# Kernel tuning notes

Measured on AMD Instinct MI355X. Metric: run time of the kernel, lower is better.

The kernel has to match this reference:

```python
import jax, jax.numpy as jnp
import numpy as np

EMBED_DIM = 1024
NUM_HEADS = 16
HEAD_DIM = EMBED_DIM // NUM_HEADS
GLOBAL_HEADS = 1
LOCAL_K = 128
SCALE = HEAD_DIM ** -0.5


def setup_inputs() -> dict:
    key = jax.random.key(0)
    ks = jax.random.split(key, 9)
    B, n = 4, 2048
    s = 1.0 / np.sqrt(EMBED_DIM)  # torch Linear default uniform(-1/sqrt(in), 1/sqrt(in))
    def lin(k):
        kw, kb = jax.random.split(k)
        W = jax.random.uniform(kw, (EMBED_DIM, EMBED_DIM), jnp.float32, -s, s)
        b = jax.random.uniform(kb, (EMBED_DIM,), jnp.float32, -s, s)
        return W, b
    wq, bq = lin(ks[0])
    wk, bk = lin(ks[1])
    wv, bv = lin(ks[2])
    wo, bo = lin(ks[3])
    x = jax.random.normal(ks[4], (B, n, EMBED_DIM), jnp.float32)
    return {"x": x, "wq": wq, "bq": bq, "wk": wk, "bk": bk,
            "wv": wv, "bv": bv, "wo": wo, "bo": bo}


def _attend(x, wq, bq, wk, bk, wv, bv, wo, bo):
    B, n, E = x.shape
    H, D = NUM_HEADS, HEAD_DIM
    def proj(W, b):
        t = x @ W.T + b                       # [B, n, E]
        return t.reshape(B, n, H, D).transpose(0, 2, 1, 3)  # [B, H, n, D]
    q, k, v = proj(wq, bq), proj(wk, bk), proj(wv, bv)
    scores = jnp.einsum('bhqd,bhkd->bhqk', q, k) * SCALE  # [B, H, n, n]
    idx = jnp.arange(n)
    band = jnp.abs(idx[:, None] - idx[None, :]) <= LOCAL_K  # [n, n] True = allowed
    is_global = jnp.arange(H) < GLOBAL_HEADS
    mask = band[None, :, :] | is_global[:, None, None]      # [H, n, n]
    scores = jnp.where(mask[None], scores, -jnp.inf)
    attn = jax.nn.softmax(scores, axis=-1)   # dropout is identity (p=0 / eval)
    out = jnp.einsum('bhqk,bhkd->bhqd', attn, v)
    out = out.transpose(0, 2, 1, 3).reshape(B, n, E)
    return out @ wo.T + bo


def reference(x, wq, bq, wk, bk, wv, bv, wo, bo):
    return _attend(x, wq, bq, wk, bk, wv, bv, wo, bo)
```

## Files before the change

### kernel.cpp

```cpp
#include <hip/hip_runtime.h>

typedef __attribute__((ext_vector_type(4))) float f32x4;
typedef __attribute__((ext_vector_type(16))) float f32x16;
typedef __attribute__((ext_vector_type(8))) short s16x8;

#define GLDS(gsrc, ldst) \
  __builtin_amdgcn_global_load_lds((const __attribute__((address_space(1))) void*)(gsrc), \
                                   (__attribute__((address_space(3))) void*)(ldst), 16, 0, 0)

__device__ __forceinline__ ushort f2bf(float f) {
  union { float f; unsigned u; } x; x.f = f;
  unsigned r = (x.u + 0x7FFFu + ((x.u >> 16) & 1u)) >> 16;
  return (ushort)r;
}

__device__ __forceinline__ float fexp2(float x) {
  float r;
  asm("v_exp_f32 %0, %1" : "=v"(r) : "v"(x));
  return r;
}

__device__ __forceinline__ uint cvtpk(float a, float b) {
  uint r;
  asm("v_cvt_pk_bf16_f32 %0, %1, %2" : "=v"(r) : "v"(a), "v"(b));
  return r;
}

__device__ __forceinline__ s16x8 mk_frag(uint x0, uint x1, uint x2, uint x3) {
  union { uint u[4]; s16x8 v; } t;
  t.u[0] = x0; t.u[1] = x1; t.u[2] = x2; t.u[3] = x3;
  return t.v;
}

__global__ __launch_bounds__(256) void castall(
    const float* __restrict__ x, const float* __restrict__ wq, const float* __restrict__ wk,
    const float* __restrict__ wv, const float* __restrict__ wo,
    ushort* __restrict__ xb, ushort* __restrict__ wqkvb, ushort* __restrict__ wob) {
  int bid = blockIdx.x;
  const float* in; ushort* op;
  if (bid < 8192)       { in = x;  op = xb; }
  else if (bid < 9216)  { in = wq; op = wqkvb;           bid -= 8192; }
  else if (bid < 10240) { in = wk; op = wqkvb + 1048576; bid -= 9216; }
  else if (bid < 11264) { in = wv; op = wqkvb + 2097152; bid -= 10240; }
  else                  { in = wo; op = wob;             bid -= 11264; }
  int i = (bid * 256 + threadIdx.x) * 4;
  float4 v = *(const float4*)(in + i);
  ushort4 r;
  r.x = f2bf(v.x); r.y = f2bf(v.y); r.z = f2bf(v.z); r.w = f2bf(v.w);
  *(ushort4*)(op + i) = r;
}

template<int OUTBF16>
__global__ __launch_bounds__(512, 2) void gemm256(
    const ushort* __restrict__ A, const ushort* __restrict__ Bt,
    const float* __restrict__ bias0, const float* __restrict__ bias1,
    const float* __restrict__ bias2,
    void* __restrict__ Cout, int M, int N, int K, int nxn)
{
  __shared__ __align__(16) ushort lds[73728];
  const int tid = threadIdx.x;
  const int w = tid >> 6, lane = tid & 63;
  const int lrow = lane & 15, lg = lane >> 4;
  const int wm = w >> 2, wn = w & 3;
  const int cpx = gridDim.x >> 3;
  const int wgid = ((int)blockIdx.x & 7) * cpx + ((int)blockIdx.x >> 3);
  const int mblk = (wgid / nxn) * 128;
  const int nblk = (wgid % nxn) * 256;
  const int NT = K >> 6;

  const int srow = tid >> 3;
  const int scol = 8 * ((tid & 7) ^ (srow & 7));
  const ushort* Abase = A + (size_t)(mblk + srow) * K + scol;
  const ushort* Bbase = Bt + (size_t)(nblk + srow) * K + scol;
  const size_t rstep = (size_t)64 * K;
  const int dA = w * 512;
  const int dB = 8192 + w * 512;

#define STAGE_A(p, bf) { \
    GLDS((p),         &lds[(bf) + dA]); \
    GLDS((p) + rstep, &lds[(bf) + dA + 4096]); }
#define STAGE_B(p, bf) { \
    GLDS((p),             &lds[(bf) + dB]); \
    GLDS((p) + rstep,     &lds[(bf) + dB + 4096]); \
    GLDS((p) + 2 * rstep, &lds[(bf) + dB + 8192]); \
    GLDS((p) + 3 * rstep, &lds[(bf) + dB + 12288]); }

  const int laneA0 = (wm * 64 + lrow) * 64 + ((lg ^ (lrow & 7)) << 3);
  const int laneA1 = (wm * 64 + lrow) * 64 + (((4 + lg) ^ (lrow & 7)) << 3);
  const int laneB0 = 8192 + (wn * 64 + lrow) * 64 + ((lg ^ (lrow & 7)) << 3);
  const int laneB1 = 8192 + (wn * 64 + lrow) * 64 + (((4 + lg) ^ (lrow & 7)) << 3);

  const f32x4 zero = {0.f, 0.f, 0.f, 0.f};
  f32x4 acc[4][4];
#pragma unroll
  for (int m = 0; m < 4; m++)
#pragma unroll
    for (int n = 0; n < 4; n++) acc[m][n] = zero;

  STAGE_A(Abase, 0); STAGE_B(Bbase, 0);
  if (NT > 1) { STAGE_A(Abase + 64, 24576); STAGE_B(Bbase + 64, 24576); }

  const ushort* aP = Abase + 128;
  const ushort* bP = Bbase + 128;
  int bb = 0, bbS = 49152;

  for (int t = 0; t < NT; ++t) {
    if (t < NT - 1) { asm volatile("s_waitcnt vmcnt(6)" ::: "memory"); }
    else            { asm volatile("s_waitcnt vmcnt(0)" ::: "memory"); }
    __builtin_amdgcn_s_barrier();
    const int pA0 = bb + laneA0, pA1 = bb + laneA1;
    const int pB0 = bb + laneB0, pB1 = bb + laneB1;
    const bool pf = (t + 2 < NT);

    if (pf) STAGE_A(aP, bbS);
    {
      s16x8 af[4], bf_[4];
#pragma unroll
      for (int m = 0; m < 4; m++) af[m] = *(const s16x8*)&lds[pA0 + m * 1024];
#pragma unroll
      for (int n = 0; n < 4; n++) bf_[n] = *(const s16x8*)&lds[pB0 + n * 1024];
      __builtin_amdgcn_s_setprio(1);
#pragma unroll
      for (int m = 0; m < 4; m++)
#pragma unroll
        for (int n = 0; n < 4; n++)
          acc[m][n] = __builtin_amdgcn_mfma_f32_16x16x32_bf16(af[m], bf_[n], acc[m][n], 0, 0, 0);
      __builtin_amdgcn_s_setprio(0);
    }
    if (pf) STAGE_B(bP, bbS);
    {
      s16x8 af[4], bf_[4];
#pragma unroll
      for (int m = 0; m < 4; m++) af[m] = *(const s16x8*)&lds[pA1 + m * 1024];
#pragma unroll
      for (int n = 0; n < 4; n++) bf_[n] = *(const s16x8*)&lds[pB1 + n * 1024];
      __builtin_amdgcn_s_setprio(1);
#pragma unroll
      for (int m = 0; m < 4; m++)
#pragma unroll
        for (int n = 0; n < 4; n++)
          acc[m][n] = __builtin_amdgcn_mfma_f32_16x16x32_bf16(af[m], bf_[n], acc[m][n], 0, 0, 0);
      __builtin_amdgcn_s_setprio(0);
    }
    if (pf) { aP += 64; bP += 64; }
    bb  = (bb  == 49152) ? 0 : bb + 24576;
    bbS = (bbS == 49152) ? 0 : bbS + 24576;
  }
#undef STAGE_A
#undef STAGE_B

  float bias_n[4];
#pragma unroll
  for (int n = 0; n < 4; n++) {
    const int col = nblk + wn * 64 + n * 16 + lrow;
    if (bias1) bias_n[n] = (col < 1024) ? bias0[col]
                          : (col < 2048 ? bias1[col - 1024] : bias2[col - 2048]);
    else bias_n[n] = bias0[col];
  }

  __syncthreads();

  if (OUTBF16) {
    ushort* Ct = lds;
#pragma unroll
    for (int m = 0; m < 4; m++)
#pragma unroll
      for (int n = 0; n < 4; n++)
#pragma unroll
        for (int i = 0; i < 4; i++)
          Ct[(wm * 64 + m * 16 + 4 * lg + i) * 256 + wn * 64 + n * 16 + lrow] =
              f2bf(acc[m][n][i] + bias_n[n]);
    __syncthreads();
    ushort* Cg = (ushort*)Cout;
#pragma unroll
    for (int r = 0; r < 8; r++) {
      const int row = r * 16 + (tid >> 5);
      const int col = (tid & 31) * 8;
      *(s16x8*)&Cg[(size_t)(mblk + row) * N + nblk + col] = *(const s16x8*)&lds[r * 4096 + tid * 8];
    }
  } else {
    float* Cf = (float*)lds;
#pragma unroll
    for (int m = 0; m < 4; m++)
#pragma unroll
      for (int n = 0; n < 4; n++)
#pragma unroll
        for (int i = 0; i < 4; i++)
          Cf[(wm * 64 + m * 16 + 4 * lg + i) * 256 + wn * 64 + n * 16 + lrow] =
              acc[m][n][i] + bias_n[n];
    __syncthreads();
    float* Cg = (float*)Cout;
#pragma unroll
    for (int r = 0; r < 16; r++) {
      const int row = r * 8 + (tid >> 6);
      const int col = (tid & 63) * 4;
      *(float4*)&Cg[(size_t)(mblk + row) * N + nblk + col] = *(const float4*)&Cf[r * 2048 + tid * 4];
    }
  }
}

__global__ __launch_bounds__(128, 2) void attn_kernel(const ushort* __restrict__ qkv,
                                                      ushort* __restrict__ outp,
                                                      float* __restrict__ oPart,
                                                      float* __restrict__ mPart,
                                                      float* __restrict__ lPart)
{
  __shared__ __align__(16) ushort Ks[2][4096];
  __shared__ __align__(16) ushort Vt[2][4096];

  const int tid = threadIdx.x;
  const int w = tid >> 6, lane = tid & 63;
  const int lq = lane & 31, hi = lane >> 5;

  const int bid = (blockIdx.x & 7) * 368 + (blockIdx.x >> 3);
  int h, b, bx, kv_lo, kv_hi, chunk = 0;
  bool isGlobal;
  if (bid < 1024) {
    isGlobal = true; h = 0;
    chunk = bid >> 7;
    int qb = bid & 127;
    b = qb >> 5; bx = qb & 31;
    kv_lo = chunk * 256; kv_hi = kv_lo + 256;
  } else {
    isGlobal = false;
    int t = bid - 1024;
    h = 1 + (t >> 7);
    int qb = t & 127;
    b = qb >> 5; bx = qb & 31;
    kv_lo = bx * 64 - 128; if (kv_lo < 0) kv_lo = 0;
    kv_hi = bx * 64 + 192; if (kv_hi > 2048) kv_hi = 2048;
  }
  const int q0b = bx * 64;
  const int q0w = q0b + w * 32;
  const int q_abs = q0w + lq;
  const ushort* Qp = qkv + (size_t)b * 2048 * 3072 + h * 64;
  const ushort* Kp = Qp + 1024;
  const ushort* Vp = Qp + 2048;

  s16x8 qf[4];
#pragma unroll
  for (int c = 0; c < 4; c++)
    qf[c] = *(const s16x8*)(Qp + (size_t)q_abs * 3072 + 16 * c + 8 * hi);

  f32x16 o0, o1;
#pragma unroll
  for (int r = 0; r < 16; r++) { o0[r] = 0.f; o1[r] = 0.f; }
  float mrun = -3e38f, lsum = 0.f;
  const float SCL = 0.18033688011112042f;

  const int kr = tid >> 3, kc = tid & 7;
  const int vsp = tid >> 3, vsg = tid & 7;
  const int kswz = 8 * (kc ^ (kr & 7));

  const ushort* vr0 = Vp + (size_t)(kv_lo + 4 * vsp) * 3072 + 8 * vsg;
  s16x8 v0 = *(const s16x8*)vr0;
  s16x8 v1 = *(const s16x8*)(vr0 + 3072);
  s16x8 v2 = *(const s16x8*)(vr0 + 6144);
  s16x8 v3 = *(const s16x8*)(vr0 + 9216);
#pragma unroll
  for (int i = 0; i < 4; i++)
    GLDS(Kp + (size_t)(kv_lo + 16 * i + kr) * 3072 + kswz, &Ks[0][i * 1024 + w * 512]);

  int buf = 0;
  for (int kv = kv_lo; kv < kv_hi; kv += 64) {
    const bool needMask = !isGlobal && (kv < q0b - 64 || kv + 64 > q0b + 128);
    const bool hasNext = (kv + 64 < kv_hi);

    s16x8 vn0, vn1, vn2, vn3;
    if (hasNext) {
      const ushort* vr = Vp + (size_t)(kv + 64 + 4 * vsp) * 3072 + 8 * vsg;
      vn0 = *(const s16x8*)vr;
      vn1 = *(const s16x8*)(vr + 3072);
      vn2 = *(const s16x8*)(vr + 6144);
      vn3 = *(const s16x8*)(vr + 9216);
    }

#pragma unroll
    for (int j = 0; j < 8; j++) {
      const int d = 8 * vsg + j;
      const int sl = ((vsp >> 1) ^ j ^ vsg) & 7;
      const int a0 = d * 64 + sl * 8 + ((4 * vsp) & 7);
      *(uint*)&Vt[buf][a0]     = (uint)(ushort)v0[j] | ((uint)(ushort)v1[j] << 16);
      *(uint*)&Vt[buf][a0 + 2] = (uint)(ushort)v2[j] | ((uint)(ushort)v3[j] << 16);
    }
    if (hasNext) asm volatile("s_waitcnt vmcnt(4)" ::: "memory");
    else         asm volatile("s_waitcnt vmcnt(0)" ::: "memory");
    asm volatile("s_waitcnt lgkmcnt(0)" ::: "memory");
    __builtin_amdgcn_s_barrier();
    if (hasNext) {
#pragma unroll
      for (int i = 0; i < 4; i++)
        GLDS(Kp + (size_t)(kv + 64 + 16 * i + kr) * 3072 + kswz, &Ks[buf ^ 1][i * 1024 + w * 512]);
    }

    f32x16 s0, s1;
#pragma unroll
    for (int r = 0; r < 16; r++) { s0[r] = 0.f; s1[r] = 0.f; }
#pragma unroll
    for (int c = 0; c < 4; c++) {
      const int gx = ((2 * c + hi) ^ (lq & 7)) << 3;
      s16x8 kf0 = *(const s16x8*)&Ks[buf][lq * 64 + gx];
      s16x8 kf1 = *(const s16x8*)&Ks[buf][(32 + lq) * 64 + gx];
      s0 = __builtin_amdgcn_mfma_f32_32x32x16_bf16(kf0, qf[c], s0, 0, 0, 0);
      s1 = __builtin_amdgcn_mfma_f32_32x32x16_bf16(kf1, qf[c], s1, 0, 0, 0);
    }

    float rm = -3e38f;
    if (needMask) {
#pragma unroll
      for (int r = 0; r < 16; r++) {
        const int kvr = kv + (r & 3) + 8 * (r >> 2) + 4 * hi;
        const int dq0 = q_abs - kvr;
        s0[r] = (dq0 <= 128 && dq0 >= -128) ? s0[r] : -3e38f;
        const int dq1 = dq0 - 32;
        s1[r] = (dq1 <= 128 && dq1 >= -128) ? s1[r] : -3e38f;
        rm = fmaxf(rm, fmaxf(s0[r], s1[r]));
      }
    } else {
#pragma unroll
      for (int r = 0; r < 16; r++) rm = fmaxf(rm, fmaxf(s0[r], s1[r]));
    }
    rm = fmaxf(rm, __shfl_xor(rm, 32)) * SCL;

    if (!__all(rm <= mrun + 8.f)) {
      float mnew = fmaxf(mrun, rm);
      float alpha = fexp2(mrun - mnew);
      mrun = mnew;
      lsum *= alpha;
#pragma unroll
      for (int r = 0; r < 16; r++) {
        float av = __shfl(alpha, (r & 3) + 8 * (r >> 2) + 4 * hi);
        o0[r] *= av; o1[r] *= av;
      }
    }

    float rs = 0.f;
#pragma unroll
    for (int r = 0; r < 16; r++) {
      s0[r] = fexp2(__builtin_fmaf(s0[r], SCL, -mrun)); rs += s0[r];
      s1[r] = fexp2(__builtin_fmaf(s1[r], SCL, -mrun)); rs += s1[r];
    }
    rs += __shfl_xor(rs, 32);
    lsum += rs;

#pragma unroll
    for (int cc = 0; cc < 4; cc++) {
      uint x0, x1, x2, x3;
      if (cc == 0) { x0 = cvtpk(s0[0], s0[1]);  x1 = cvtpk(s0[2], s0[3]);
                     x2 = cvtpk(s0[4], s0[5]);  x3 = cvtpk(s0[6], s0[7]); }
      else if (cc == 1) { x0 = cvtpk(s0[8], s0[9]);   x1 = cvtpk(s0[10], s0[11]);
                          x2 = cvtpk(s0[12], s0[13]); x3 = cvtpk(s0[14], s0[15]); }
      else if (cc == 2) { x0 = cvtpk(s1[0], s1[1]);  x1 = cvtpk(s1[2], s1[3]);
                          x2 = cvtpk(s1[4], s1[5]);  x3 = cvtpk(s1[6], s1[7]); }
      else { x0 = cvtpk(s1[8], s1[9]);   x1 = cvtpk(s1[10], s1[11]);
             x2 = cvtpk(s1[12], s1[13]); x3 = cvtpk(s1[14], s1[15]); }
      uint t0 = hi ? x0 : x2;
      uint t1 = hi ? x1 : x3;
      uint r0 = __shfl_xor(t0, 32);
      uint r1 = __shfl_xor(t1, 32);
      uint w0 = hi ? r0 : x0;
      uint w1 = hi ? r1 : x1;
      uint w2 = hi ? x2 : r0;
      uint w3 = hi ? x3 : r1;
      s16x8 pa = mk_frag(w0, w1, w2, w3);
#pragma unroll
      for (int db = 0; db < 2; db++) {
        const int d = 32 * db + lq;
        s16x8 vf = *(const s16x8*)&Vt[buf][d * 64 +
            ((((2 * cc + hi) ^ (d & 7) ^ (d >> 3)) & 7) << 3)];
        if (db == 0) o0 = __builtin_amdgcn_mfma_f32_32x32x16_bf16(pa, vf, o0, 0, 0, 0);
        else         o1 = __builtin_amdgcn_mfma_f32_32x32x16_bf16(pa, vf, o1, 0, 0, 0);
      }
    }

    v0 = vn0; v1 = vn1; v2 = vn2; v3 = vn3;
    buf ^= 1;
  }

  if (isGlobal) {
    const size_t rq = (size_t)(chunk * 4 + b) * 2048 + q0w;
    if (hi == 0) {
      mPart[rq + lq] = mrun;
      lPart[rq + lq] = lsum;
    }
#pragma unroll
    for (int r = 0; r < 16; r++) {
      const int qr = (r & 3) + 8 * (r >> 2) + 4 * hi;
      oPart[(rq + qr) * 64 + lq]      = o0[r];
      oPart[(rq + qr) * 64 + 32 + lq] = o1[r];
    }
  } else {
    float linv = 1.f / lsum;
#pragma unroll
    for (int r = 0; r < 16; r++) {
      const int qr = (r & 3) + 8 * (r >> 2) + 4 * hi;
      float iv = __shfl(linv, qr);
      size_t orow = (size_t)(b * 2048 + q0w + qr) * 1024 + h * 64;
      outp[orow + lq]      = f2bf(o0[r] * iv);
      outp[orow + 32 + lq] = f2bf(o1[r] * iv);
    }
  }
}

__global__ __launch_bounds__(256) void combine_kernel(const float* __restrict__ oPart,
                                                      const float* __restrict__ mPart,
                                                      const float* __restrict__ lPart,
                                                      ushort* __restrict__ attno) {
  const int tid = threadIdx.x;
  const int row = blockIdx.x * 64 + (tid >> 2);
  const int d0 = (tid & 3) * 16;
  float m[8], l[8], M = -3e38f;
#pragma unroll
  for (int p = 0; p < 8; p++) {
    m[p] = mPart[p * 8192 + row];
    l[p] = lPart[p * 8192 + row];
    M = fmaxf(M, m[p]);
  }
  float L = 0.f, wgt[8];
#pragma unroll
  for (int p = 0; p < 8; p++) { wgt[p] = fexp2(m[p] - M); L += wgt[p] * l[p]; }
  float inv = 1.f / L;
  float acc[16];
#pragma unroll
  for (int j = 0; j < 16; j++) acc[j] = 0.f;
#pragma unroll
  for (int p = 0; p < 8; p++) {
    const float* op = oPart + ((size_t)p * 8192 + row) * 64 + d0;
    float wv = wgt[p];
#pragma unroll
    for (int j = 0; j < 16; j += 4) {
      float4 v = *(const float4*)(op + j);
      acc[j]     += wv * v.x; acc[j + 1] += wv * v.y;
      acc[j + 2] += wv * v.z; acc[j + 3] += wv * v.w;
    }
  }
  ushort* dst = attno + (size_t)row * 1024 + d0;
#pragma unroll
  for (int j = 0; j < 16; j++) dst[j] = f2bf(acc[j] * inv);
}

extern "C" void kernel_launch(void* const* d_in, const int* in_sizes, int n_in,
                              void* d_out, int out_size, void* d_ws, size_t ws_size,
                              hipStream_t stream) {
  const float* x  = (const float*)d_in[0];
  const float* wq = (const float*)d_in[1];
  const float* bq = (const float*)d_in[2];
  const float* wk = (const float*)d_in[3];
  const float* bk = (const float*)d_in[4];
  const float* wv = (const float*)d_in[5];
  const float* bv = (const float*)d_in[6];
  const float* wo = (const float*)d_in[7];
  const float* bo = (const float*)d_in[8];

  char* ws = (char*)d_ws;
  ushort* xb    = (ushort*)(ws);
  ushort* wqkvb = (ushort*)(ws + 16777216);
  ushort* wob   = (ushort*)(ws + 23068672);
  ushort* qkvb  = (ushort*)(ws + 25165824);
  ushort* attno = (ushort*)(ws + 75497472);
  float* oPart = (float*)(ws);
  float* mPart = (float*)(ws + 16777216);
  float* lPart = (float*)(ws + 16777216 + 262144);

  castall<<<12288, 256, 0, stream>>>(x, wq, wk, wv, wo, xb, wqkvb, wob);

  gemm256<1><<<768, 512, 0, stream>>>(xb, wqkvb, bq, bk, bv,
                                      (void*)qkvb, 8192, 3072, 1024, 12);

  attn_kernel<<<2944, 128, 0, stream>>>(qkvb, attno, oPart, mPart, lPart);
  combine_kernel<<<128, 256, 0, stream>>>(oPart, mPart, lPart, attno);

  gemm256<0><<<256, 512, 0, stream>>>(attno, wob, bo, nullptr, nullptr,
                                      (void*)d_out, 8192, 1024, 1024, 4);
}
```

Baseline: 159.0 us.

## Grow attention block to 128 queries with 4 waves sharing K/V tiles

The attention kernel now uses 256-thread blocks covering 128 query rows (four waves of 32) instead of 64, halving the grid. Each K/V tile staged in LDS is shared by twice as many queries, which cuts redundant global loads and LDS staging per query. Waves skip the compute for KV tiles outside their own band window via a per-wave active flag. The trade-off is that the union band per block is wider (384 keys), so some waves idle at barriers while others compute, and occupancy per CU changes with the larger blocks.

```diff
diff --git a/kernel.cpp b/kernel.cpp
--- a/kernel.cpp
+++ b/kernel.cpp
@@ -199,7 +199,7 @@
   }
 }
 
-__global__ __launch_bounds__(128, 2) void attn_kernel(const ushort* __restrict__ qkv,
+__global__ __launch_bounds__(256, 2) void attn_kernel(const ushort* __restrict__ qkv,
                                                       ushort* __restrict__ outp,
                                                       float* __restrict__ oPart,
                                                       float* __restrict__ mPart,
@@ -211,28 +211,29 @@
   const int tid = threadIdx.x;
   const int w = tid >> 6, lane = tid & 63;
   const int lq = lane & 31, hi = lane >> 5;
-
-  const int bid = (blockIdx.x & 7) * 368 + (blockIdx.x >> 3);
+  const float NINF = -__builtin_inff();
+
+  const int bid = (blockIdx.x & 7) * 184 + (blockIdx.x >> 3);
   int h, b, bx, kv_lo, kv_hi, chunk = 0;
   bool isGlobal;
-  if (bid < 1024) {
+  if (bid < 512) {
     isGlobal = true; h = 0;
-    chunk = bid >> 7;
-    int qb = bid & 127;
-    b = qb >> 5; bx = qb & 31;
+    chunk = bid >> 6;
+    int qb = bid & 63;
+    b = qb >> 4; bx = qb & 15;
     kv_lo = chunk * 256; kv_hi = kv_lo + 256;
   } else {
     isGlobal = false;
-    int t = bid - 1024;
-    h = 1 + (t >> 7);
-    int qb = t & 127;
-    b = qb >> 5; bx = qb & 31;
-    kv_lo = bx * 64 - 128; if (kv_lo < 0) kv_lo = 0;
-    kv_hi = bx * 64 + 192; if (kv_hi > 2048) kv_hi = 2048;
-  }
-  const int q0b = bx * 64;
-  const int q0w = q0b + w * 32;
-  const int q_abs = q0w + lq;
+    int t = bid - 512;
+    h = 1 + (t >> 6);
+    int qb = t & 63;
+    b = qb >> 4; bx = qb & 15;
+    kv_lo = bx * 128 - 128; if (kv_lo < 0) kv_lo = 0;
+    kv_hi = bx * 128 + 256; if (kv_hi > 2048) kv_hi = 2048;
+  }
+  const int q0blk = bx * 128;
+  const int qw = q0blk + 32 * w;
+  const int q_abs = qw + lq;
   const ushort* Qp = qkv + (size_t)b * 2048 * 3072 + h * 64;
   const ushort* Kp = Qp + 1024;
   const ushort* Vp = Qp + 2048;
@@ -248,137 +249,135 @@
   float mrun = -3e38f, lsum = 0.f;
   const float SCL = 0.18033688011112042f;
 
-  const int kr = tid >> 3, kc = tid & 7;
-  const int vsp = tid >> 3, vsg = tid & 7;
-  const int kswz = 8 * (kc ^ (kr & 7));
-
-  const ushort* vr0 = Vp + (size_t)(kv_lo + 4 * vsp) * 3072 + 8 * vsg;
+  const int kg = lane >> 3;
+  const int kswz = 8 * ((lane & 7) ^ kg);
+  const int krow0 = 16 * w + kg;
+  const int vsp = tid >> 3;
+  const int vsg = tid & 7;
+
+  const ushort* vr0 = Vp + (size_t)(kv_lo + 2 * vsp) * 3072 + 8 * vsg;
   s16x8 v0 = *(const s16x8*)vr0;
   s16x8 v1 = *(const s16x8*)(vr0 + 3072);
-  s16x8 v2 = *(const s16x8*)(vr0 + 6144);
-  s16x8 v3 = *(const s16x8*)(vr0 + 9216);
-#pragma unroll
-  for (int i = 0; i < 4; i++)
-    GLDS(Kp + (size_t)(kv_lo + 16 * i + kr) * 3072 + kswz, &Ks[0][i * 1024 + w * 512]);
+  GLDS(Kp + (size_t)(kv_lo + krow0) * 3072 + kswz,     &Ks[0][(2 * w) * 512]);
+  GLDS(Kp + (size_t)(kv_lo + krow0 + 8) * 3072 + kswz, &Ks[0][(2 * w + 1) * 512]);
 
   int buf = 0;
   for (int kv = kv_lo; kv < kv_hi; kv += 64) {
-    const bool needMask = !isGlobal && (kv < q0b - 64 || kv + 64 > q0b + 128);
     const bool hasNext = (kv + 64 < kv_hi);
-
-    s16x8 vn0, vn1, vn2, vn3;
+    const bool active = isGlobal || ((kv + 63 >= qw - 128) && (kv <= qw + 159));
+    const bool needMask = !isGlobal && active && ((kv < qw - 97) || (kv > qw + 65));
+
+    s16x8 vn0, vn1;
     if (hasNext) {
-      const ushort* vr = Vp + (size_t)(kv + 64 + 4 * vsp) * 3072 + 8 * vsg;
+      const ushort* vr = Vp + (size_t)(kv + 64 + 2 * vsp) * 3072 + 8 * vsg;
       vn0 = *(const s16x8*)vr;
       vn1 = *(const s16x8*)(vr + 3072);
-      vn2 = *(const s16x8*)(vr + 6144);
-      vn3 = *(const s16x8*)(vr + 9216);
     }
 
 #pragma unroll
     for (int j = 0; j < 8; j++) {
       const int d = 8 * vsg + j;
-      const int sl = ((vsp >> 1) ^ j ^ vsg) & 7;
-      const int a0 = d * 64 + sl * 8 + ((4 * vsp) & 7);
-      *(uint*)&Vt[buf][a0]     = (uint)(ushort)v0[j] | ((uint)(ushort)v1[j] << 16);
-      *(uint*)&Vt[buf][a0 + 2] = (uint)(ushort)v2[j] | ((uint)(ushort)v3[j] << 16);
-    }
-    if (hasNext) asm volatile("s_waitcnt vmcnt(4)" ::: "memory");
+      const int sl = ((vsp >> 2) ^ j ^ vsg) & 7;
+      *(uint*)&Vt[buf][d * 64 + sl * 8 + ((2 * vsp) & 7)] =
+          (uint)(ushort)v0[j] | ((uint)(ushort)v1[j] << 16);
+    }
+    if (hasNext) asm volatile("s_waitcnt vmcnt(2)" ::: "memory");
     else         asm volatile("s_waitcnt vmcnt(0)" ::: "memory");
     asm volatile("s_waitcnt lgkmcnt(0)" ::: "memory");
     __builtin_amdgcn_s_barrier();
     if (hasNext) {
-#pragma unroll
-      for (int i = 0; i < 4; i++)
-        GLDS(Kp + (size_t)(kv + 64 + 16 * i + kr) * 3072 + kswz, &Ks[buf ^ 1][i * 1024 + w * 512]);
-    }
-
-    f32x16 s0, s1;
-#pragma unroll
-    for (int r = 0; r < 16; r++) { s0[r] = 0.f; s1[r] = 0.f; }
-#pragma unroll
-    for (int c = 0; c < 4; c++) {
-      const int gx = ((2 * c + hi) ^ (lq & 7)) << 3;
-      s16x8 kf0 = *(const s16x8*)&Ks[buf][lq * 64 + gx];
-      s16x8 kf1 = *(const s16x8*)&Ks[buf][(32 + lq) * 64 + gx];
-      s0 = __builtin_amdgcn_mfma_f32_32x32x16_bf16(kf0, qf[c], s0, 0, 0, 0);
-      s1 = __builtin_amdgcn_mfma_f32_32x32x16_bf16(kf1, qf[c], s1, 0, 0, 0);
-    }
-
-    float rm = -3e38f;
-    if (needMask) {
+      GLDS(Kp + (size_t)(kv + 64 + krow0) * 3072 + kswz,     &Ks[buf ^ 1][(2 * w) * 512]);
+      GLDS(Kp + (size_t)(kv + 64 + krow0 + 8) * 3072 + kswz, &Ks[buf ^ 1][(2 * w + 1) * 512]);
+    }
+
+    if (active) {
+      f32x16 s0, s1;
+#pragma unroll
+      for (int r = 0; r < 16; r++) { s0[r] = 0.f; s1[r] = 0.f; }
+#pragma unroll
+      for (int c = 0; c < 4; c++) {
+        const int gx = ((2 * c + hi) ^ (lq & 7)) << 3;
+        s16x8 kf0 = *(const s16x8*)&Ks[buf][lq * 64 + gx];
+        s16x8 kf1 = *(const s16x8*)&Ks[buf][(32 + lq) * 64 + gx];
+        s0 = __builtin_amdgcn_mfma_f32_32x32x16_bf16(kf0, qf[c], s0, 0, 0, 0);
+        s1 = __builtin_amdgcn_mfma_f32_32x32x16_bf16(kf1, qf[c], s1, 0, 0, 0);
+      }
+
+      float rm = NINF;
+      if (needMask) {
+#pragma unroll
+        for (int r = 0; r < 16; r++) {
+          const int kvr = kv + (r & 3) + 8 * (r >> 2) + 4 * hi;
+          const int dq0 = q_abs - kvr;
+          s0[r] = (dq0 <= 128 && dq0 >= -128) ? s0[r] : NINF;
+          const int dq1 = dq0 - 32;
+          s1[r] = (dq1 <= 128 && dq1 >= -128) ? s1[r] : NINF;
+          rm = fmaxf(rm, fmaxf(s0[r], s1[r]));
+        }
+      } else {
+#pragma unroll
+        for (int r = 0; r < 16; r++) rm = fmaxf(rm, fmaxf(s0[r], s1[r]));
+      }
+      rm = fmaxf(rm, __shfl_xor(rm, 32)) * SCL;
+
+      if (!__all(rm <= mrun + 8.f)) {
+        float mnew = fmaxf(mrun, rm);
+        float alpha = fexp2(mrun - mnew);
+        mrun = mnew;
+        lsum *= alpha;
+#pragma unroll
+        for (int r = 0; r < 16; r++) {
+          float av = __shfl(alpha, (r & 3) + 8 * (r >> 2) + 4 * hi);
+          o0[r] *= av; o1[r] *= av;
+        }
+      }
+
+      float rs = 0.f;
 #pragma unroll
       for (int r = 0; r < 16; r++) {
-        const int kvr = kv + (r & 3) + 8 * (r >> 2) + 4 * hi;
-        const int dq0 = q_abs - kvr;
-        s0[r] = (dq0 <= 128 && dq0 >= -128) ? s0[r] : -3e38f;
-        const int dq1 = dq0 - 32;
-        s1[r] = (dq1 <= 128 && dq1 >= -128) ? s1[r] : -3e38f;
-        rm = fmaxf(rm, fmaxf(s0[r], s1[r]));
+        s0[r] = fexp2(__builtin_fmaf(s0[r], SCL, -mrun)); rs += s0[r];
+        s1[r] = fexp2(__builtin_fmaf(s1[r], SCL, -mrun)); rs += s1[r];
       }
-    } else {
-#pragma unroll
-      for (int r = 0; r < 16; r++) rm = fmaxf(rm, fmaxf(s0[r], s1[r]));
-    }
-    rm = fmaxf(rm, __shfl_xor(rm, 32)) * SCL;
-
-    if (!__all(rm <= mrun + 8.f)) {
-      float mnew = fmaxf(mrun, rm);
-      float alpha = fexp2(mrun - mnew);
-      mrun = mnew;
-      lsum *= alpha;
-#pragma unroll
-      for (int r = 0; r < 16; r++) {
-        float av = __shfl(alpha, (r & 3) + 8 * (r >> 2) + 4 * hi);
-        o0[r] *= av; o1[r] *= av;
+      rs += __shfl_xor(rs, 32);
+      lsum += rs;
+
+#pragma unroll
+      for (int cc = 0; cc < 4; cc++) {
+        uint x0, x1, x2, x3;
+        if (cc == 0) { x0 = cvtpk(s0[0], s0[1]);  x1 = cvtpk(s0[2], s0[3]);
+                       x2 = cvtpk(s0[4], s0[5]);  x3 = cvtpk(s0[6], s0[7]); }
+        else if (cc == 1) { x0 = cvtpk(s0[8], s0[9]);   x1 = cvtpk(s0[10], s0[11]);
+                            x2 = cvtpk(s0[12], s0[13]); x3 = cvtpk(s0[14], s0[15]); }
+        else if (cc == 2) { x0 = cvtpk(s1[0], s1[1]);  x1 = cvtpk(s1[2], s1[3]);
+                            x2 = cvtpk(s1[4], s1[5]);  x3 = cvtpk(s1[6], s1[7]); }
+        else { x0 = cvtpk(s1[8], s1[9]);   x1 = cvtpk(s1[10], s1[11]);
+               x2 = cvtpk(s1[12], s1[13]); x3 = cvtpk(s1[14], s1[15]); }
+        uint t0 = hi ? x0 : x2;
+        uint t1 = hi ? x1 : x3;
+        uint r0 = __shfl_xor(t0, 32);
+        uint r1 = __shfl_xor(t1, 32);
+        uint w0 = hi ? r0 : x0;
+        uint w1 = hi ? r1 : x1;
+        uint w2 = hi ? x2 : r0;
+        uint w3 = hi ? x3 : r1;
+        s16x8 pa = mk_frag(w0, w1, w2, w3);
+#pragma unroll
+        for (int db = 0; db < 2; db++) {
+          const int d = 32 * db + lq;
+          s16x8 vf = *(const s16x8*)&Vt[buf][d * 64 +
+              ((((2 * cc + hi) ^ (d & 7) ^ (d >> 3)) & 7) << 3)];
+          if (db == 0) o0 = __builtin_amdgcn_mfma_f32_32x32x16_bf16(pa, vf, o0, 0, 0, 0);
+          else         o1 = __builtin_amdgcn_mfma_f32_32x32x16_bf16(pa, vf, o1, 0, 0, 0);
+        }
       }
     }
 
-    float rs = 0.f;
-#pragma unroll
-    for (int r = 0; r < 16; r++) {
-      s0[r] = fexp2(__builtin_fmaf(s0[r], SCL, -mrun)); rs += s0[r];
-      s1[r] = fexp2(__builtin_fmaf(s1[r], SCL, -mrun)); rs += s1[r];
-    }
-    rs += __shfl_xor(rs, 32);
-    lsum += rs;
-
-#pragma unroll
-    for (int cc = 0; cc < 4; cc++) {
-      uint x0, x1, x2, x3;
-      if (cc == 0) { x0 = cvtpk(s0[0], s0[1]);  x1 = cvtpk(s0[2], s0[3]);
-                     x2 = cvtpk(s0[4], s0[5]);  x3 = cvtpk(s0[6], s0[7]); }
-      else if (cc == 1) { x0 = cvtpk(s0[8], s0[9]);   x1 = cvtpk(s0[10], s0[11]);
-                          x2 = cvtpk(s0[12], s0[13]); x3 = cvtpk(s0[14], s0[15]); }
-      else if (cc == 2) { x0 = cvtpk(s1[0], s1[1]);  x1 = cvtpk(s1[2], s1[3]);
-                          x2 = cvtpk(s1[4], s1[5]);  x3 = cvtpk(s1[6], s1[7]); }
-      else { x0 = cvtpk(s1[8], s1[9]);   x1 = cvtpk(s1[10], s1[11]);
-             x2 = cvtpk(s1[12], s1[13]); x3 = cvtpk(s1[14], s1[15]); }
-      uint t0 = hi ? x0 : x2;
-      uint t1 = hi ? x1 : x3;
-      uint r0 = __shfl_xor(t0, 32);
-      uint r1 = __shfl_xor(t1, 32);
-      uint w0 = hi ? r0 : x0;
-      uint w1 = hi ? r1 : x1;
-      uint w2 = hi ? x2 : r0;
-      uint w3 = hi ? x3 : r1;
-      s16x8 pa = mk_frag(w0, w1, w2, w3);
-#pragma unroll
-      for (int db = 0; db < 2; db++) {
-        const int d = 32 * db + lq;
-        s16x8 vf = *(const s16x8*)&Vt[buf][d * 64 +
-            ((((2 * cc + hi) ^ (d & 7) ^ (d >> 3)) & 7) << 3)];
-        if (db == 0) o0 = __builtin_amdgcn_mfma_f32_32x32x16_bf16(pa, vf, o0, 0, 0, 0);
-        else         o1 = __builtin_amdgcn_mfma_f32_32x32x16_bf16(pa, vf, o1, 0, 0, 0);
-      }
-    }
-
-    v0 = vn0; v1 = vn1; v2 = vn2; v3 = vn3;
+    v0 = vn0; v1 = vn1;
     buf ^= 1;
   }
 
   if (isGlobal) {
-    const size_t rq = (size_t)(chunk * 4 + b) * 2048 + q0w;
+    const size_t rq = (size_t)(chunk * 4 + b) * 2048 + qw;
     if (hi == 0) {
       mPart[rq + lq] = mrun;
       lPart[rq + lq] = lsum;
@@ -395,7 +394,7 @@
     for (int r = 0; r < 16; r++) {
       const int qr = (r & 3) + 8 * (r >> 2) + 4 * hi;
       float iv = __shfl(linv, qr);
-      size_t orow = (size_t)(b * 2048 + q0w + qr) * 1024 + h * 64;
+      size_t orow = (size_t)(b * 2048 + qw + qr) * 1024 + h * 64;
       outp[orow + lq]      = f2bf(o0[r] * iv);
       outp[orow + 32 + lq] = f2bf(o1[r] * iv);
     }
@@ -467,7 +466,7 @@
   gemm256<1><<<768, 512, 0, stream>>>(xb, wqkvb, bq, bk, bv,
                                       (void*)qkvb, 8192, 3072, 1024, 12);
 
-  attn_kernel<<<2944, 128, 0, stream>>>(qkvb, attno, oPart, mPart, lPart);
+  attn_kernel<<<1472, 256, 0, stream>>>(qkvb, attno, oPart, mPart, lPart);
   combine_kernel<<<128, 256, 0, stream>>>(oPart, mPart, lPart, attno);
 
   gemm256<0><<<256, 512, 0, stream>>>(attno, wob, bo, nullptr, nullptr,
```

Result: faster. 153.2 us (median of 2 runs) (-3.7%).
